# Kernel tuning notes

Hardware: AMD Instinct MI355X
Metric: run time of the kernel (lower is better)

## Reference

```python
import jax, jax.numpy as jnp
import numpy as np

B, M, F_N, D, GS, L = 32, 512, 64, 128, 4, 8  # batch, max atoms, in feats, int_d, graph channels, layers


def setup_inputs() -> dict:
    key = jax.random.key(0)
    ks = jax.random.split(key, 8)
    G = jax.random.uniform(ks[0], (B, GS, M, M), dtype=jnp.float32)      # dense multi-channel adjacency
    x = jax.random.normal(ks[1], (B, M, F_N), dtype=jnp.float32)          # per-atom features
    W0 = jax.random.normal(ks[2], (GS, F_N, D), dtype=jnp.float32) * 0.05 # per-channel Linear, layer 0
    b0 = jax.random.normal(ks[3], (GS, D), dtype=jnp.float32) * 0.05
    Wl = jax.random.normal(ks[4], (L - 1, GS, D, D), dtype=jnp.float32) * 0.05
    bl = jax.random.normal(ks[5], (L - 1, GS, D), dtype=jnp.float32) * 0.05
    Wout = jax.random.normal(ks[6], (D, 1), dtype=jnp.float32) * 0.05
    bout = jax.random.normal(ks[7], (1,), dtype=jnp.float32) * 0.05
    return {"G": G, "x": x, "W0": W0, "b0": b0, "Wl": Wl, "bl": bl, "Wout": Wout, "bout": bout}


def _graph_mat_layer(G, h, W, b):
    # per-channel linear: [B,M,C] x [GS,C,P] -> [B,GS,M,P]
    multi = jnp.einsum('bmc,gcp->bgmp', h, W) + b[None, :, None, :]
    # per-sample, per-channel adjacency matmul: [B,GS,M,M] @ [B,GS,M,P]
    xout = jnp.einsum('bgmn,bgnp->bgmp', G, multi)
    # ReLU then goodmax aggregation over graph channels (dim=1)
    return jnp.max(jax.nn.relu(xout), axis=1)  # [B,M,P]


def reference(G, x, W0, b0, Wl, bl, Wout, bout):
    # layer 0: input width F_N != D, so no residual (shape mismatch)
    h = _graph_mat_layer(G, x, W0, b0)
    # layers 1..L-1: resnet skip (shapes match)
    for i in range(L - 1):
        h = _graph_mat_layer(G, h, Wl[i], bl[i]) + h
    # lin_out on [B,M,D] -> [B,M,1]
    return h @ Wout + bout
```

## Files before the change

kernel.cpp:

```cpp
#include <hip/hip_runtime.h>
#include <stdint.h>


#define B_  32
#define M_  512
#define FN_ 64
#define D_  128
#define GS_ 4
#define L_  8

typedef __attribute__((ext_vector_type(8))) short short8;
typedef __attribute__((ext_vector_type(4))) float f32x4;
typedef unsigned short us;

__device__ __forceinline__ us f2bf(float f) {
  union { float f; unsigned int u; } v; v.f = f;
  return (us)((v.u + 0x7FFFu + ((v.u >> 16) & 1u)) >> 16);
}

__device__ __forceinline__ void gl16(const void* g, void* l) {
  __builtin_amdgcn_global_load_lds((const __attribute__((address_space(1))) void*)g,
                                   (__attribute__((address_space(3))) void*)l, 16, 0, 0);
}

__global__ void k_conv(const float4* __restrict__ src, ushort4* __restrict__ dst, int n4) {
  int i = blockIdx.x * blockDim.x + threadIdx.x;
  int st = gridDim.x * blockDim.x;
  for (; i < n4; i += st) {
    float4 v = src[i];
    ushort4 o;
    o.x = f2bf(v.x); o.y = f2bf(v.y); o.z = f2bf(v.z); o.w = f2bf(v.w);
    dst[i] = o;
  }
}

__global__ void k_convW(const float* __restrict__ W0, const float* __restrict__ Wl,
                        us* __restrict__ W0bT, us* __restrict__ WlbT) {
  int i = blockIdx.x * blockDim.x + threadIdx.x;
  const int n0 = GS_ * FN_ * D_;
  if (i < n0) {
    int g = i / (FN_ * D_), r = i % (FN_ * D_), c = r / D_, p = r % D_;
    W0bT[((size_t)g * D_ + p) * FN_ + c] = f2bf(W0[i]);
  } else {
    int j = i - n0;
    if (j < 7 * GS_ * D_ * D_) {
      int l = j / (GS_ * D_ * D_), r = j % (GS_ * D_ * D_);
      int g = r / (D_ * D_), r2 = r % (D_ * D_), c = r2 / D_, p = r2 % D_;
      WlbT[(((size_t)l * GS_ + g) * D_ + p) * D_ + c] = f2bf(Wl[j]);
    }
  }
}

template<int NK>
__launch_bounds__(256)
__global__ void k_lin(const us* __restrict__ A0, const us* __restrict__ B0,
                      int aRS, int aSB, int bSG,
                      us* __restrict__ outBf, const float* __restrict__ bias) {
  __shared__ __align__(16) us sm[2][2][4096];
  const int t = threadIdx.x;
  const int bid = blockIdx.x;
  const int mt = bid & 3, g = (bid >> 2) & 3, b = bid >> 4;
  const us* Ap = A0 + (size_t)b * aSB + (size_t)mt * 128 * aRS;
  const us* Bp = B0 + (size_t)g * bSG;

  const int tr = t >> 2;
  const int tcs = ((t & 3) ^ ((t >> 3) & 3)) * 8;

  {
    const us* ga = Ap + (size_t)tr * aRS + tcs;
    const us* gb = Bp + (size_t)tr * aRS + tcs;
    gl16(ga, &sm[0][0][t * 8]);
    gl16(ga + (size_t)64 * aRS, &sm[0][0][2048 + t * 8]);
    gl16(gb, &sm[0][1][t * 8]);
    gl16(gb + (size_t)64 * aRS, &sm[0][1][2048 + t * 8]);
  }

  const int lane = t & 63;
  const int wm = ((t >> 7) & 1) * 64;
  const int wp = ((t >> 6) & 1) * 64;
  const int lr = lane & 15;
  const int kk = (((lane >> 4) ^ ((lane >> 1) & 3))) * 8;

  f32x4 acc[4][4];
#pragma unroll
  for (int i = 0; i < 4; ++i)
#pragma unroll
    for (int j = 0; j < 4; ++j) acc[i][j] = (f32x4){0.f, 0.f, 0.f, 0.f};

  int cur = 0;
  for (int ks = 0; ks < NK; ++ks) {
    __syncthreads();
    if (ks + 1 < NK) {
      const int nb = cur ^ 1;
      const us* ga = Ap + (size_t)(ks + 1) * 32 + (size_t)tr * aRS + tcs;
      const us* gb = Bp + (size_t)(ks + 1) * 32 + (size_t)tr * aRS + tcs;
      gl16(ga, &sm[nb][0][t * 8]);
      gl16(ga + (size_t)64 * aRS, &sm[nb][0][2048 + t * 8]);
      gl16(gb, &sm[nb][1][t * 8]);
      gl16(gb + (size_t)64 * aRS, &sm[nb][1][2048 + t * 8]);
    }
    const us* sa = sm[cur][0];
    const us* sb = sm[cur][1];
    short8 af[4], bfr[4];
#pragma unroll
    for (int i = 0; i < 4; ++i)
      af[i] = *(const short8*)&sa[(wm + i * 16 + lr) * 32 + kk];
#pragma unroll
    for (int j = 0; j < 4; ++j)
      bfr[j] = *(const short8*)&sb[(wp + j * 16 + lr) * 32 + kk];
#pragma unroll
    for (int i = 0; i < 4; ++i)
#pragma unroll
      for (int j = 0; j < 4; ++j)
        acc[i][j] = __builtin_amdgcn_mfma_f32_16x16x32_bf16(af[i], bfr[j], acc[i][j], 0, 0, 0);
    cur ^= 1;
  }

  const int rb = (lane >> 4) * 4;
#pragma unroll
  for (int j = 0; j < 4; ++j) {
    const int p = wp + j * 16 + lr;
    const float bv = bias[g * D_ + p];
    us* op = outBf + ((size_t)(b * GS_ + g) * D_ + p) * M_;
#pragma unroll
    for (int i = 0; i < 4; ++i) {
      const int n = mt * 128 + wm + i * 16 + rb;
      f32x4 v = acc[i][j];
      ushort4 o;
      o.x = f2bf(v[0] + bv); o.y = f2bf(v[1] + bv);
      o.z = f2bf(v[2] + bv); o.w = f2bf(v[3] + bv);
      *(ushort4*)(op + n) = o;
    }
  }
}

template<int FIRST, int LAST>
__launch_bounds__(512, 2)
__global__ void k_fused(const us* __restrict__ Gh, const us* __restrict__ MhT,
                        float* __restrict__ h, us* __restrict__ hb,
                        const float* __restrict__ Wout, const float* __restrict__ bout,
                        float* __restrict__ out) {
  __shared__ __align__(16) us sm[3 * 24576];
  const int bid = blockIdx.x;
  const int swz = (bid & 7) * 32 + (bid >> 3);
  const int b = swz >> 3, mt = swz & 7;

  const int t = threadIdx.x;
  const int w = t >> 6;
  const int g = w >> 1;
  const int hf = w & 1;
  const int lane = t & 63;
  const int lr = lane & 15;
  const int kq = lane >> 4;

  const us* AgB = Gh + ((size_t)(b * GS_ + g) * M_ + mt * 64) * M_;
  const us* BgB = MhT + (size_t)(b * GS_ + g) * D_ * M_;
  const int srow = lane >> 2;
  const int scol = ((lane & 3) ^ ((lane >> 3) & 3)) * 8;
  const int s0 = hf * 6;

#define STAGE(bufi, ks) do { \
    us* bb_ = sm + (bufi) * 24576 + g * 6144; \
    _Pragma("unroll") \
    for (int u_ = 0; u_ < 6; ++u_) { \
      const int ls_ = s0 + u_; \
      const us* src_ = (ls_ < 4) \
        ? AgB + (size_t)(ls_ * 16 + srow) * M_ + (ks) * 32 + scol \
        : BgB + (size_t)((ls_ - 4) * 16 + srow) * M_ + (ks) * 32 + scol; \
      gl16(src_, bb_ + ls_ * 512 + lane * 8); \
    } \
  } while (0)

  f32x4 acc[4][4];
#pragma unroll
  for (int i = 0; i < 4; ++i)
#pragma unroll
    for (int j = 0; j < 4; ++j) acc[i][j] = (f32x4){0.f, 0.f, 0.f, 0.f};

  STAGE(0, 0);
  STAGE(1, 1);

  const int kk = ((kq ^ ((lr >> 1) & 3))) * 8;

#pragma unroll
  for (int ks = 0; ks < 16; ++ks) {
    if (ks < 15) asm volatile("s_waitcnt vmcnt(6)" ::: "memory");
    else         asm volatile("s_waitcnt vmcnt(0)" ::: "memory");
    __builtin_amdgcn_s_barrier();
    __builtin_amdgcn_sched_barrier(0);
    const us* sa = sm + (ks % 3) * 24576 + g * 6144;
    const us* sb = sa + 2048;
    short8 af[4], bf[4];
#pragma unroll
    for (int i = 0; i < 4; ++i)
      af[i] = *(const short8*)&sa[(i * 16 + lr) * 32 + kk];
#pragma unroll
    for (int j = 0; j < 4; ++j)
      bf[j] = *(const short8*)&sb[(hf * 64 + j * 16 + lr) * 32 + kk];
    if (ks + 2 < 16) STAGE((ks + 2) % 3, ks + 2);
    asm volatile("s_waitcnt lgkmcnt(0)" ::: "memory");
    __builtin_amdgcn_sched_barrier(0);
#pragma unroll
    for (int i = 0; i < 4; ++i)
#pragma unroll
      for (int j = 0; j < 4; ++j)
        acc[i][j] = __builtin_amdgcn_mfma_f32_16x16x32_bf16(af[i], bf[j], acc[i][j], 0, 0, 0);
  }
#undef STAGE

  __builtin_amdgcn_s_barrier();
  __builtin_amdgcn_sched_barrier(0);

  {
    float* red = (float*)sm + (size_t)g * 8192;
#pragma unroll
    for (int i = 0; i < 4; ++i)
#pragma unroll
      for (int j = 0; j < 4; ++j) {
        const int col = hf * 64 + j * 16 + lr;
        const int ch = col >> 2, cw = col & 3;
#pragma unroll
        for (int cc = 0; cc < 4; ++cc) {
          const int row = i * 16 + kq * 4 + cc;
          red[row * 128 + ((ch ^ (row & 7)) << 2) + cw] = fmaxf(acc[i][j][cc], 0.f);
        }
      }
  }
  __builtin_amdgcn_s_barrier();
  __builtin_amdgcn_sched_barrier(0);

  {
    const int m_l = t >> 3, pq = t & 7;
    const float* red = (const float*)sm;
    float4 vm[4];
#pragma unroll
    for (int k = 0; k < 4; ++k) {
      const int ch = pq * 4 + k;
      const float* rp = red + (size_t)m_l * 128 + ((ch ^ (m_l & 7)) << 2);
      float4 v = *(const float4*)rp;
#pragma unroll
      for (int gg = 1; gg < 4; ++gg) {
        float4 u = *(const float4*)(rp + (size_t)gg * 8192);
        v.x = fmaxf(v.x, u.x); v.y = fmaxf(v.y, u.y);
        v.z = fmaxf(v.z, u.z); v.w = fmaxf(v.w, u.w);
      }
      vm[k] = v;
    }
    const size_t ho = ((size_t)b * M_ + mt * 64 + m_l) * D_ + pq * 16;
    float4* hp = (float4*)(h + ho);
    if (!FIRST) {
#pragma unroll
      for (int k = 0; k < 4; ++k) {
        float4 hv = hp[k];
        vm[k].x += hv.x; vm[k].y += hv.y; vm[k].z += hv.z; vm[k].w += hv.w;
      }
    }
    if constexpr (!LAST) {
      ushort4* hbp = (ushort4*)(hb + ho);
#pragma unroll
      for (int k = 0; k < 4; ++k) {
        float4 v = vm[k];
        hp[k] = v;
        ushort4 o;
        o.x = f2bf(v.x); o.y = f2bf(v.y); o.z = f2bf(v.z); o.w = f2bf(v.w);
        hbp[k] = o;
      }
    } else {
      float s = 0.f;
#pragma unroll
      for (int k = 0; k < 4; ++k) {
        const float4 wv = *(const float4*)(Wout + pq * 16 + k * 4);
        s += vm[k].x * wv.x + vm[k].y * wv.y + vm[k].z * wv.z + vm[k].w * wv.w;
      }
      s += __shfl_xor(s, 1);
      s += __shfl_xor(s, 2);
      s += __shfl_xor(s, 4);
      if (pq == 0) out[(size_t)b * M_ + mt * 64 + m_l] = s + bout[0];
    }
  }
}

extern "C" void kernel_launch(void* const* d_in, const int* in_sizes, int n_in,
                              void* d_out, int out_size, void* d_ws, size_t ws_size,
                              hipStream_t stream) {
  const float* G    = (const float*)d_in[0];
  const float* x    = (const float*)d_in[1];
  const float* W0   = (const float*)d_in[2];
  const float* b0   = (const float*)d_in[3];
  const float* Wl   = (const float*)d_in[4];
  const float* bl   = (const float*)d_in[5];
  const float* Wout = (const float*)d_in[6];
  const float* bout = (const float*)d_in[7];

  char* ws = (char*)d_ws;
  us*    Gh   = (us*)(ws);
  us*    MhT  = (us*)(ws + 67108864);
  float* h    = (float*)(ws + 83886080);
  us*    hb   = (us*)(ws + 92274688);
  us*    xb   = (us*)(ws + 96468992);
  us*    W0bT = (us*)(ws + 98566144);
  us*    WlbT = (us*)(ws + 98631680);

  k_conv<<<2048, 256, 0, stream>>>((const float4*)G, (ushort4*)Gh, (B_ * GS_ * M_ * M_) / 4);
  k_conv<<<1024, 256, 0, stream>>>((const float4*)x, (ushort4*)xb, (B_ * M_ * FN_) / 4);
  k_convW<<<1920, 256, 0, stream>>>(W0, Wl, W0bT, WlbT);

  k_lin<FN_ / 32><<<512, 256, 0, stream>>>(xb, W0bT, FN_, M_ * FN_, D_ * FN_, MhT, b0);
  k_fused<1, 0><<<256, 512, 0, stream>>>(Gh, MhT, h, hb, Wout, bout, (float*)d_out);

  for (int l = 1; l < L_ - 1; ++l) {
    k_lin<D_ / 32><<<512, 256, 0, stream>>>(hb, WlbT + (size_t)(l - 1) * GS_ * D_ * D_,
        D_, M_ * D_, D_ * D_, MhT, bl + (size_t)(l - 1) * GS_ * D_);
    k_fused<0, 0><<<256, 512, 0, stream>>>(Gh, MhT, h, hb, Wout, bout, (float*)d_out);
  }

  k_lin<D_ / 32><<<512, 256, 0, stream>>>(hb, WlbT + (size_t)(L_ - 2) * GS_ * D_ * D_,
      D_, M_ * D_, D_ * D_, MhT, bl + (size_t)(L_ - 2) * GS_ * D_);
  k_fused<0, 1><<<256, 512, 0, stream>>>(Gh, MhT, h, hb, Wout, bout, (float*)d_out);
}
```

Baseline: 314.3 us.

## Fuse all layers into one persistent kernel with per-batch flag synchronization

Replaces the chain of per-layer linear and adjacency kernels, plus the separate G/x conversion kernels, with a single persistent kernel of 256 blocks. Each block converts its own G tile and x rows, keeps h in registers and its bf16 copy in LDS, and computes the per-channel linear from LDS. The eight blocks of a sample sync through atomic flags before the adjacency matmul. This removes launch overhead and the global round trips of h/hb, at the cost of a spin-wait barrier that relies on all 256 blocks being co-resident, and of lower occupancy (1 block per CU).

```diff
diff --git a/kernel.cpp b/kernel.cpp
--- a/kernel.cpp
+++ b/kernel.cpp
@@ -23,259 +23,284 @@
                                    (__attribute__((address_space(3))) void*)l, 16, 0, 0);
 }
 
-__global__ void k_conv(const float4* __restrict__ src, ushort4* __restrict__ dst, int n4) {
-  int i = blockIdx.x * blockDim.x + threadIdx.x;
-  int st = gridDim.x * blockDim.x;
-  for (; i < n4; i += st) {
-    float4 v = src[i];
-    ushort4 o;
-    o.x = f2bf(v.x); o.y = f2bf(v.y); o.z = f2bf(v.z); o.w = f2bf(v.w);
-    dst[i] = o;
-  }
-}
-
 __global__ void k_convW(const float* __restrict__ W0, const float* __restrict__ Wl,
-                        us* __restrict__ W0bT, us* __restrict__ WlbT) {
+                        us* __restrict__ W0T, us* __restrict__ WlT) {
   int i = blockIdx.x * blockDim.x + threadIdx.x;
   const int n0 = GS_ * FN_ * D_;
   if (i < n0) {
     int g = i / (FN_ * D_), r = i % (FN_ * D_), c = r / D_, p = r % D_;
-    W0bT[((size_t)g * D_ + p) * FN_ + c] = f2bf(W0[i]);
+    W0T[((size_t)g * D_ + p) * FN_ + c] = f2bf(W0[i]);
   } else {
     int j = i - n0;
     if (j < 7 * GS_ * D_ * D_) {
       int l = j / (GS_ * D_ * D_), r = j % (GS_ * D_ * D_);
       int g = r / (D_ * D_), r2 = r % (D_ * D_), c = r2 / D_, p = r2 % D_;
-      WlbT[(((size_t)l * GS_ + g) * D_ + p) * D_ + c] = f2bf(Wl[j]);
-    }
-  }
-}
-
-template<int NK>
-__launch_bounds__(256)
-__global__ void k_lin(const us* __restrict__ A0, const us* __restrict__ B0,
-                      int aRS, int aSB, int bSG,
-                      us* __restrict__ outBf, const float* __restrict__ bias) {
-  __shared__ __align__(16) us sm[2][2][4096];
-  const int t = threadIdx.x;
-  const int bid = blockIdx.x;
-  const int mt = bid & 3, g = (bid >> 2) & 3, b = bid >> 4;
-  const us* Ap = A0 + (size_t)b * aSB + (size_t)mt * 128 * aRS;
-  const us* Bp = B0 + (size_t)g * bSG;
-
-  const int tr = t >> 2;
-  const int tcs = ((t & 3) ^ ((t >> 3) & 3)) * 8;
-
-  {
-    const us* ga = Ap + (size_t)tr * aRS + tcs;
-    const us* gb = Bp + (size_t)tr * aRS + tcs;
-    gl16(ga, &sm[0][0][t * 8]);
-    gl16(ga + (size_t)64 * aRS, &sm[0][0][2048 + t * 8]);
-    gl16(gb, &sm[0][1][t * 8]);
-    gl16(gb + (size_t)64 * aRS, &sm[0][1][2048 + t * 8]);
-  }
-
-  const int lane = t & 63;
-  const int wm = ((t >> 7) & 1) * 64;
-  const int wp = ((t >> 6) & 1) * 64;
-  const int lr = lane & 15;
-  const int kk = (((lane >> 4) ^ ((lane >> 1) & 3))) * 8;
-
+      WlT[(((size_t)l * GS_ + g) * D_ + p) * D_ + c] = f2bf(Wl[j]);
+    }
+  }
+}
+
+__global__ void k_init(int* flags) { flags[threadIdx.x] = 0; }
+
+template<int NKA, int CC>
+__device__ __forceinline__ void stageA(const us* __restrict__ Wt,
+                                       const float* __restrict__ bias,
+                                       us* __restrict__ Mw,
+                                       const us* hbL, us (*smS)[24576],
+                                       int g, int hf, int lr, int kq,
+                                       int srow, int scol, int kk, int b, int mt) {
   f32x4 acc[4][4];
 #pragma unroll
   for (int i = 0; i < 4; ++i)
 #pragma unroll
     for (int j = 0; j < 4; ++j) acc[i][j] = (f32x4){0.f, 0.f, 0.f, 0.f};
 
-  int cur = 0;
-  for (int ks = 0; ks < NK; ++ks) {
-    __syncthreads();
-    if (ks + 1 < NK) {
-      const int nb = cur ^ 1;
-      const us* ga = Ap + (size_t)(ks + 1) * 32 + (size_t)tr * aRS + tcs;
-      const us* gb = Bp + (size_t)(ks + 1) * 32 + (size_t)tr * aRS + tcs;
-      gl16(ga, &sm[nb][0][t * 8]);
-      gl16(ga + (size_t)64 * aRS, &sm[nb][0][2048 + t * 8]);
-      gl16(gb, &sm[nb][1][t * 8]);
-      gl16(gb + (size_t)64 * aRS, &sm[nb][1][2048 + t * 8]);
-    }
-    const us* sa = sm[cur][0];
-    const us* sb = sm[cur][1];
-    short8 af[4], bfr[4];
+#define STGA(bufi, ks) do { \
+    us* bb_ = smS[bufi] + g * 6144; \
+    _Pragma("unroll") \
+    for (int u_ = 0; u_ < 4; ++u_) { \
+      const us* sp_ = Wt + (size_t)g * D_ * CC + (size_t)(hf * 64 + u_ * 16 + srow) * CC \
+                      + (ks) * 32 + scol; \
+      gl16(sp_, bb_ + 2048 + (hf * 4 + u_) * 512); \
+    } \
+  } while (0)
+
+  STGA(0, 0);
+  STGA(1, 1);
+  const int cm = (CC == 64) ? 7 : 15;
+#pragma unroll
+  for (int ks = 0; ks < NKA; ++ks) {
+    if (ks < NKA - 1) asm volatile("s_waitcnt vmcnt(4)" ::: "memory");
+    else              asm volatile("s_waitcnt vmcnt(0)" ::: "memory");
+    __builtin_amdgcn_sched_barrier(0);
+    const us* sb = smS[ks % 3] + g * 6144 + 2048;
+    short8 af[4], bf[4];
 #pragma unroll
     for (int i = 0; i < 4; ++i)
-      af[i] = *(const short8*)&sa[(wm + i * 16 + lr) * 32 + kk];
+      af[i] = *(const short8*)&hbL[(i * 16 + lr) * 128 + (((ks * 4 + kq) ^ (lr & cm)) << 3)];
 #pragma unroll
     for (int j = 0; j < 4; ++j)
-      bfr[j] = *(const short8*)&sb[(wp + j * 16 + lr) * 32 + kk];
+      bf[j] = *(const short8*)&sb[(hf * 64 + j * 16 + lr) * 32 + kk];
+    if (ks + 2 < NKA) STGA((ks + 2) % 3, ks + 2);
+    asm volatile("s_waitcnt lgkmcnt(0)" ::: "memory");
+    __builtin_amdgcn_sched_barrier(0);
 #pragma unroll
     for (int i = 0; i < 4; ++i)
 #pragma unroll
       for (int j = 0; j < 4; ++j)
-        acc[i][j] = __builtin_amdgcn_mfma_f32_16x16x32_bf16(af[i], bfr[j], acc[i][j], 0, 0, 0);
-    cur ^= 1;
-  }
-
-  const int rb = (lane >> 4) * 4;
+        acc[i][j] = __builtin_amdgcn_mfma_f32_16x16x32_bf16(af[i], bf[j], acc[i][j], 0, 0, 0);
+  }
+#undef STGA
+
 #pragma unroll
   for (int j = 0; j < 4; ++j) {
-    const int p = wp + j * 16 + lr;
+    const int p = hf * 64 + j * 16 + lr;
     const float bv = bias[g * D_ + p];
-    us* op = outBf + ((size_t)(b * GS_ + g) * D_ + p) * M_;
+    us* op = Mw + ((size_t)(b * GS_ + g) * D_ + p) * M_;
 #pragma unroll
     for (int i = 0; i < 4; ++i) {
-      const int n = mt * 128 + wm + i * 16 + rb;
+      const int n0 = mt * 64 + i * 16 + kq * 4;
       f32x4 v = acc[i][j];
       ushort4 o;
       o.x = f2bf(v[0] + bv); o.y = f2bf(v[1] + bv);
       o.z = f2bf(v[2] + bv); o.w = f2bf(v[3] + bv);
-      *(ushort4*)(op + n) = o;
-    }
-  }
-}
-
-template<int FIRST, int LAST>
-__launch_bounds__(512, 2)
-__global__ void k_fused(const us* __restrict__ Gh, const us* __restrict__ MhT,
-                        float* __restrict__ h, us* __restrict__ hb,
-                        const float* __restrict__ Wout, const float* __restrict__ bout,
-                        float* __restrict__ out) {
-  __shared__ __align__(16) us sm[3 * 24576];
+      *(ushort4*)(op + n0) = o;
+    }
+  }
+}
+
+__launch_bounds__(512, 1)
+__global__ void k_net(const float* __restrict__ G, const float* __restrict__ x,
+                      const us* __restrict__ W0T, const us* __restrict__ WlT,
+                      const float* __restrict__ b0, const float* __restrict__ bl,
+                      const float* __restrict__ Wout, const float* __restrict__ bout,
+                      us* __restrict__ Gh, us* __restrict__ Mh0, us* __restrict__ Mh1,
+                      int* flags, float* __restrict__ out) {
+  __shared__ __align__(16) us smS[3][24576];
+  __shared__ __align__(16) us hbL[8192];
+
   const int bid = blockIdx.x;
   const int swz = (bid & 7) * 32 + (bid >> 3);
   const int b = swz >> 3, mt = swz & 7;
 
   const int t = threadIdx.x;
-  const int w = t >> 6;
-  const int g = w >> 1;
-  const int hf = w & 1;
-  const int lane = t & 63;
-  const int lr = lane & 15;
-  const int kq = lane >> 4;
-
-  const us* AgB = Gh + ((size_t)(b * GS_ + g) * M_ + mt * 64) * M_;
-  const us* BgB = MhT + (size_t)(b * GS_ + g) * D_ * M_;
+  const int w = t >> 6, g = w >> 1, hf = w & 1;
+  const int lane = t & 63, lr = lane & 15, kq = lane >> 4;
   const int srow = lane >> 2;
   const int scol = ((lane & 3) ^ ((lane >> 3) & 3)) * 8;
-  const int s0 = hf * 6;
-
-#define STAGE(bufi, ks) do { \
-    us* bb_ = sm + (bufi) * 24576 + g * 6144; \
-    _Pragma("unroll") \
-    for (int u_ = 0; u_ < 6; ++u_) { \
-      const int ls_ = s0 + u_; \
-      const us* src_ = (ls_ < 4) \
-        ? AgB + (size_t)(ls_ * 16 + srow) * M_ + (ks) * 32 + scol \
-        : BgB + (size_t)((ls_ - 4) * 16 + srow) * M_ + (ks) * 32 + scol; \
-      gl16(src_, bb_ + ls_ * 512 + lane * 8); \
-    } \
-  } while (0)
-
-  f32x4 acc[4][4];
-#pragma unroll
-  for (int i = 0; i < 4; ++i)
-#pragma unroll
-    for (int j = 0; j < 4; ++j) acc[i][j] = (f32x4){0.f, 0.f, 0.f, 0.f};
-
-  STAGE(0, 0);
-  STAGE(1, 1);
-
-  const int kk = ((kq ^ ((lr >> 1) & 3))) * 8;
-
-#pragma unroll
-  for (int ks = 0; ks < 16; ++ks) {
-    if (ks < 15) asm volatile("s_waitcnt vmcnt(6)" ::: "memory");
-    else         asm volatile("s_waitcnt vmcnt(0)" ::: "memory");
-    __builtin_amdgcn_s_barrier();
-    __builtin_amdgcn_sched_barrier(0);
-    const us* sa = sm + (ks % 3) * 24576 + g * 6144;
-    const us* sb = sa + 2048;
-    short8 af[4], bf[4];
-#pragma unroll
-    for (int i = 0; i < 4; ++i)
-      af[i] = *(const short8*)&sa[(i * 16 + lr) * 32 + kk];
-#pragma unroll
-    for (int j = 0; j < 4; ++j)
-      bf[j] = *(const short8*)&sb[(hf * 64 + j * 16 + lr) * 32 + kk];
-    if (ks + 2 < 16) STAGE((ks + 2) % 3, ks + 2);
-    asm volatile("s_waitcnt lgkmcnt(0)" ::: "memory");
-    __builtin_amdgcn_sched_barrier(0);
-#pragma unroll
-    for (int i = 0; i < 4; ++i)
-#pragma unroll
-      for (int j = 0; j < 4; ++j)
-        acc[i][j] = __builtin_amdgcn_mfma_f32_16x16x32_bf16(af[i], bf[j], acc[i][j], 0, 0, 0);
-  }
-#undef STAGE
-
-  __builtin_amdgcn_s_barrier();
-  __builtin_amdgcn_sched_barrier(0);
+  const int kk = (kq ^ ((lr >> 1) & 3)) * 8;
+  const int m_l = t >> 3, pq = t & 7;
 
   {
-    float* red = (float*)sm + (size_t)g * 8192;
-#pragma unroll
-    for (int i = 0; i < 4; ++i)
-#pragma unroll
-      for (int j = 0; j < 4; ++j) {
-        const int col = hf * 64 + j * 16 + lr;
-        const int ch = col >> 2, cw = col & 3;
-#pragma unroll
-        for (int cc = 0; cc < 4; ++cc) {
-          const int row = i * 16 + kq * 4 + cc;
-          red[row * 128 + ((ch ^ (row & 7)) << 2) + cw] = fmaxf(acc[i][j][cc], 0.f);
+    const int segb = t >> 7, col = (t & 127) * 4;
+#pragma unroll 4
+    for (int it = 0; it < 64; ++it) {
+      const int seg = segb + it * 4;
+      const int gg = seg >> 6, rr = seg & 63;
+      const size_t rb = ((size_t)(b * GS_ + gg) * M_ + mt * 64 + rr) * M_;
+      float4 v = *(const float4*)(G + rb + col);
+      ushort4 o;
+      o.x = f2bf(v.x); o.y = f2bf(v.y); o.z = f2bf(v.z); o.w = f2bf(v.w);
+      *(ushort4*)(Gh + rb + col) = o;
+    }
+  }
+  {
+    const int row = t >> 3, c8 = t & 7;
+    const float* xs = x + ((size_t)b * M_ + mt * 64 + row) * FN_ + c8 * 8;
+    float4 v0 = *(const float4*)xs, v1 = *(const float4*)(xs + 4);
+    ushort4 o0, o1;
+    o0.x = f2bf(v0.x); o0.y = f2bf(v0.y); o0.z = f2bf(v0.z); o0.w = f2bf(v0.w);
+    o1.x = f2bf(v1.x); o1.y = f2bf(v1.y); o1.z = f2bf(v1.z); o1.w = f2bf(v1.w);
+    us* dp = hbL + row * 128 + ((c8 ^ (row & 7)) << 3);
+    *(ushort4*)dp = o0; *(ushort4*)(dp + 4) = o1;
+  }
+  __syncthreads();
+
+  f32x4 hreg[4];
+
+  for (int l = 0; l < L_; ++l) {
+    us* Mw = (l & 1) ? Mh1 : Mh0;
+
+    if (l == 0)
+      stageA<FN_ / 32, FN_>(W0T, b0, Mw, hbL, smS, g, hf, lr, kq, srow, scol, kk, b, mt);
+    else
+      stageA<D_ / 32, D_>(WlT + (size_t)(l - 1) * GS_ * D_ * D_,
+                          bl + (size_t)(l - 1) * GS_ * D_,
+                          Mw, hbL, smS, g, hf, lr, kq, srow, scol, kk, b, mt);
+
+    __builtin_amdgcn_fence(__ATOMIC_RELEASE, "agent");
+    __syncthreads();
+    if (t == 0) {
+      int* fl = flags + l * B_ + b;
+      __hip_atomic_fetch_add(fl, 1, __ATOMIC_RELAXED, __HIP_MEMORY_SCOPE_AGENT);
+      while (__hip_atomic_load(fl, __ATOMIC_RELAXED, __HIP_MEMORY_SCOPE_AGENT) < 8)
+        __builtin_amdgcn_s_sleep(2);
+    }
+    __syncthreads();
+    __builtin_amdgcn_fence(__ATOMIC_ACQUIRE, "agent");
+
+    {
+      const us* AgB = Gh + ((size_t)(b * GS_ + g) * M_ + mt * 64) * M_;
+      const us* BgB = Mw + (size_t)(b * GS_ + g) * D_ * M_;
+      f32x4 acc[4][4];
+#pragma unroll
+      for (int i = 0; i < 4; ++i)
+#pragma unroll
+        for (int j = 0; j < 4; ++j) acc[i][j] = (f32x4){0.f, 0.f, 0.f, 0.f};
+
+#define STGB(bufi, ks) do { \
+      us* bb_ = smS[bufi] + g * 6144; \
+      _Pragma("unroll") \
+      for (int u_ = 0; u_ < 6; ++u_) { \
+        const int ls_ = hf * 6 + u_; \
+        const us* sp_ = (ls_ < 4) \
+          ? AgB + (size_t)(ls_ * 16 + srow) * M_ + (ks) * 32 + scol \
+          : BgB + (size_t)((ls_ - 4) * 16 + srow) * M_ + (ks) * 32 + scol; \
+        gl16(sp_, bb_ + ls_ * 512 + lane * 8); \
+      } \
+    } while (0)
+
+      STGB(0, 0);
+      STGB(1, 1);
+#pragma unroll
+      for (int ks = 0; ks < 16; ++ks) {
+        if (ks < 15) asm volatile("s_waitcnt vmcnt(6)" ::: "memory");
+        else         asm volatile("s_waitcnt vmcnt(0)" ::: "memory");
+        __builtin_amdgcn_s_barrier();
+        __builtin_amdgcn_sched_barrier(0);
+        const us* sa = smS[ks % 3] + g * 6144;
+        const us* sb = sa + 2048;
+        short8 af[4], bf[4];
+#pragma unroll
+        for (int i = 0; i < 4; ++i)
+          af[i] = *(const short8*)&sa[(i * 16 + lr) * 32 + kk];
+#pragma unroll
+        for (int j = 0; j < 4; ++j)
+          bf[j] = *(const short8*)&sb[(hf * 64 + j * 16 + lr) * 32 + kk];
+        if (ks + 2 < 16) STGB((ks + 2) % 3, ks + 2);
+        asm volatile("s_waitcnt lgkmcnt(0)" ::: "memory");
+        __builtin_amdgcn_sched_barrier(0);
+#pragma unroll
+        for (int i = 0; i < 4; ++i)
+#pragma unroll
+          for (int j = 0; j < 4; ++j)
+            acc[i][j] = __builtin_amdgcn_mfma_f32_16x16x32_bf16(af[i], bf[j], acc[i][j], 0, 0, 0);
+      }
+#undef STGB
+
+      __builtin_amdgcn_s_barrier();
+      __builtin_amdgcn_sched_barrier(0);
+
+      {
+        float* red = (float*)smS + (size_t)g * 8192;
+#pragma unroll
+        for (int i = 0; i < 4; ++i)
+#pragma unroll
+          for (int j = 0; j < 4; ++j) {
+            const int col = hf * 64 + j * 16 + lr;
+            const int ch = col >> 2, cw = col & 3;
+#pragma unroll
+            for (int cc = 0; cc < 4; ++cc) {
+              const int row = i * 16 + kq * 4 + cc;
+              red[row * 128 + ((ch ^ (row & 7)) << 2) + cw] = fmaxf(acc[i][j][cc], 0.f);
+            }
+          }
+      }
+      __builtin_amdgcn_s_barrier();
+      __builtin_amdgcn_sched_barrier(0);
+
+      {
+        const float* red = (const float*)smS;
+        f32x4 vm[4];
+#pragma unroll
+        for (int k = 0; k < 4; ++k) {
+          const int ch = pq * 4 + k;
+          const float* rp = red + (size_t)m_l * 128 + ((ch ^ (m_l & 7)) << 2);
+          f32x4 v = *(const f32x4*)rp;
+#pragma unroll
+          for (int gg = 1; gg < 4; ++gg) {
+            f32x4 u = *(const f32x4*)(rp + (size_t)gg * 8192);
+            v[0] = fmaxf(v[0], u[0]); v[1] = fmaxf(v[1], u[1]);
+            v[2] = fmaxf(v[2], u[2]); v[3] = fmaxf(v[3], u[3]);
+          }
+          vm[k] = v;
+        }
+        if (l == 0) {
+#pragma unroll
+          for (int k = 0; k < 4; ++k) hreg[k] = vm[k];
+        } else {
+#pragma unroll
+          for (int k = 0; k < 4; ++k) {
+            hreg[k][0] += vm[k][0]; hreg[k][1] += vm[k][1];
+            hreg[k][2] += vm[k][2]; hreg[k][3] += vm[k][3];
+          }
         }
       }
-  }
-  __builtin_amdgcn_s_barrier();
-  __builtin_amdgcn_sched_barrier(0);
-
-  {
-    const int m_l = t >> 3, pq = t & 7;
-    const float* red = (const float*)sm;
-    float4 vm[4];
-#pragma unroll
-    for (int k = 0; k < 4; ++k) {
-      const int ch = pq * 4 + k;
-      const float* rp = red + (size_t)m_l * 128 + ((ch ^ (m_l & 7)) << 2);
-      float4 v = *(const float4*)rp;
-#pragma unroll
-      for (int gg = 1; gg < 4; ++gg) {
-        float4 u = *(const float4*)(rp + (size_t)gg * 8192);
-        v.x = fmaxf(v.x, u.x); v.y = fmaxf(v.y, u.y);
-        v.z = fmaxf(v.z, u.z); v.w = fmaxf(v.w, u.w);
+      __builtin_amdgcn_s_barrier();
+
+      if (l < L_ - 1) {
+        us* d0 = hbL + m_l * 128 + (((2 * pq) ^ (m_l & 15)) << 3);
+        us* d1 = hbL + m_l * 128 + (((2 * pq + 1) ^ (m_l & 15)) << 3);
+        ushort4 o0, o1, o2, o3;
+        o0.x = f2bf(hreg[0][0]); o0.y = f2bf(hreg[0][1]); o0.z = f2bf(hreg[0][2]); o0.w = f2bf(hreg[0][3]);
+        o1.x = f2bf(hreg[1][0]); o1.y = f2bf(hreg[1][1]); o1.z = f2bf(hreg[1][2]); o1.w = f2bf(hreg[1][3]);
+        o2.x = f2bf(hreg[2][0]); o2.y = f2bf(hreg[2][1]); o2.z = f2bf(hreg[2][2]); o2.w = f2bf(hreg[2][3]);
+        o3.x = f2bf(hreg[3][0]); o3.y = f2bf(hreg[3][1]); o3.z = f2bf(hreg[3][2]); o3.w = f2bf(hreg[3][3]);
+        *(ushort4*)d0 = o0; *(ushort4*)(d0 + 4) = o1;
+        *(ushort4*)d1 = o2; *(ushort4*)(d1 + 4) = o3;
+        __syncthreads();
+      } else {
+        float s = 0.f;
+#pragma unroll
+        for (int k = 0; k < 4; ++k) {
+          const float4 wv = *(const float4*)(Wout + pq * 16 + k * 4);
+          s += hreg[k][0] * wv.x + hreg[k][1] * wv.y + hreg[k][2] * wv.z + hreg[k][3] * wv.w;
+        }
+        s += __shfl_xor(s, 1);
+        s += __shfl_xor(s, 2);
+        s += __shfl_xor(s, 4);
+        if (pq == 0) out[(size_t)b * M_ + mt * 64 + m_l] = s + bout[0];
       }
-      vm[k] = v;
-    }
-    const size_t ho = ((size_t)b * M_ + mt * 64 + m_l) * D_ + pq * 16;
-    float4* hp = (float4*)(h + ho);
-    if (!FIRST) {
-#pragma unroll
-      for (int k = 0; k < 4; ++k) {
-        float4 hv = hp[k];
-        vm[k].x += hv.x; vm[k].y += hv.y; vm[k].z += hv.z; vm[k].w += hv.w;
-      }
-    }
-    if constexpr (!LAST) {
-      ushort4* hbp = (ushort4*)(hb + ho);
-#pragma unroll
-      for (int k = 0; k < 4; ++k) {
-        float4 v = vm[k];
-        hp[k] = v;
-        ushort4 o;
-        o.x = f2bf(v.x); o.y = f2bf(v.y); o.z = f2bf(v.z); o.w = f2bf(v.w);
-        hbp[k] = o;
-      }
-    } else {
-      float s = 0.f;
-#pragma unroll
-      for (int k = 0; k < 4; ++k) {
-        const float4 wv = *(const float4*)(Wout + pq * 16 + k * 4);
-        s += vm[k].x * wv.x + vm[k].y * wv.y + vm[k].z * wv.z + vm[k].w * wv.w;
-      }
-      s += __shfl_xor(s, 1);
-      s += __shfl_xor(s, 2);
-      s += __shfl_xor(s, 4);
-      if (pq == 0) out[(size_t)b * M_ + mt * 64 + m_l] = s + bout[0];
     }
   }
 }
@@ -293,28 +318,15 @@
   const float* bout = (const float*)d_in[7];
 
   char* ws = (char*)d_ws;
-  us*    Gh   = (us*)(ws);
-  us*    MhT  = (us*)(ws + 67108864);
-  float* h    = (float*)(ws + 83886080);
-  us*    hb   = (us*)(ws + 92274688);
-  us*    xb   = (us*)(ws + 96468992);
-  us*    W0bT = (us*)(ws + 98566144);
-  us*    WlbT = (us*)(ws + 98631680);
-
-  k_conv<<<2048, 256, 0, stream>>>((const float4*)G, (ushort4*)Gh, (B_ * GS_ * M_ * M_) / 4);
-  k_conv<<<1024, 256, 0, stream>>>((const float4*)x, (ushort4*)xb, (B_ * M_ * FN_) / 4);
-  k_convW<<<1920, 256, 0, stream>>>(W0, Wl, W0bT, WlbT);
-
-  k_lin<FN_ / 32><<<512, 256, 0, stream>>>(xb, W0bT, FN_, M_ * FN_, D_ * FN_, MhT, b0);
-  k_fused<1, 0><<<256, 512, 0, stream>>>(Gh, MhT, h, hb, Wout, bout, (float*)d_out);
-
-  for (int l = 1; l < L_ - 1; ++l) {
-    k_lin<D_ / 32><<<512, 256, 0, stream>>>(hb, WlbT + (size_t)(l - 1) * GS_ * D_ * D_,
-        D_, M_ * D_, D_ * D_, MhT, bl + (size_t)(l - 1) * GS_ * D_);
-    k_fused<0, 0><<<256, 512, 0, stream>>>(Gh, MhT, h, hb, Wout, bout, (float*)d_out);
-  }
-
-  k_lin<D_ / 32><<<512, 256, 0, stream>>>(hb, WlbT + (size_t)(L_ - 2) * GS_ * D_ * D_,
-      D_, M_ * D_, D_ * D_, MhT, bl + (size_t)(L_ - 2) * GS_ * D_);
-  k_fused<0, 1><<<256, 512, 0, stream>>>(Gh, MhT, h, hb, Wout, bout, (float*)d_out);
-}
+  us*   Gh    = (us*)(ws);
+  us*   Mh0   = (us*)(ws + 67108864);
+  us*   Mh1   = (us*)(ws + 83886080);
+  us*   W0T   = (us*)(ws + 100663296);
+  us*   WlT   = (us*)(ws + 100663296 + 65536);
+  int*  flags = (int*)(ws + 102760448);
+
+  k_convW<<<1920, 256, 0, stream>>>(W0, Wl, W0T, WlT);
+  k_init<<<1, 256, 0, stream>>>(flags);
+  k_net<<<256, 512, 0, stream>>>(G, x, W0T, WlT, b0, bl, Wout, bout,
+                                 Gh, Mh0, Mh1, flags, (float*)d_out);
+}
```

Measured after the change: 986.9 us. 214% more time.
